# Optimization experiments

Hardware: AMD Instinct MI355X
Metric: run time of the kernel (lower is better)

Reference implementation:

```python
import jax, jax.numpy as jnp
import numpy as np

N_NODES = 100000
N_EDGES = 800000
IN_DIM, HID_DIM, OUT_DIM = 128, 256, 40


def setup_inputs() -> dict:
    key = jax.random.key(0)
    ks = jax.random.split(key, 8)
    x = jax.random.normal(ks[0], (N_NODES, IN_DIM), dtype=jnp.float32)
    edge_index = jax.random.randint(ks[1], (2, N_EDGES), 0, N_NODES, dtype=jnp.int64)
    # PyG SAGEConv params: lin_l (neighbor path, with bias), lin_r (root path, no bias)
    def glorot(k, fan_in, fan_out):
        lim = np.sqrt(6.0 / (fan_in + fan_out)).astype(np.float32)
        return jax.random.uniform(k, (fan_in, fan_out), jnp.float32, -lim, lim)
    W1l = glorot(ks[2], IN_DIM, HID_DIM)
    W1r = glorot(ks[3], IN_DIM, HID_DIM)
    b1 = jnp.zeros((HID_DIM,), jnp.float32)
    W2l = glorot(ks[4], HID_DIM, OUT_DIM)
    W2r = glorot(ks[5], HID_DIM, OUT_DIM)
    b2 = jnp.zeros((OUT_DIM,), jnp.float32)
    return {"x": x, "edge_index": edge_index, "W1l": W1l, "b1": b1, "W1r": W1r,
            "W2l": W2l, "b2": b2, "W2r": W2r}


def _sage_conv(x, src, dst, Wl, b, Wr, n_nodes):
    # mean aggregation of neighbor features: gather x[src], scatter-add to dst, divide by degree
    msg = x[src]                                              # [E, D]
    agg = jax.ops.segment_sum(msg, dst, num_segments=n_nodes)  # [N, D]
    cnt = jax.ops.segment_sum(jnp.ones((src.shape[0],), x.dtype), dst,
                              num_segments=n_nodes)            # [N]
    agg = agg / jnp.maximum(cnt, 1.0)[:, None]
    # out = lin_l(mean_agg) + lin_r(x)  (lin_l carries the bias in PyG)
    return agg @ Wl + b + x @ Wr


def reference(x, edge_index, W1l, b1, W1r, W2l, b2, W2r):
    src, dst = edge_index[0], edge_index[1]
    n = x.shape[0]
    h = _sage_conv(x, src, dst, W1l, b1, W1r, n)
    h = jax.nn.relu(h)
    # F.dropout(training=self.training): identity at inference
    out = _sage_conv(h, src, dst, W2l, b2, W2r, n)
    return out
```

## Files before the change

kernel.cpp:

```cpp
#include <hip/hip_runtime.h>
#include <hip/hip_bf16.h>


#define NN   100000
#define NNP  100096
#define NE   800000
#define NB1  391
#define NCHK 32
#define ECH  25000
#define NSLI 16
#define NSL  6250

typedef unsigned short ushortT;
typedef __attribute__((ext_vector_type(8))) short bf16x8;
typedef __attribute__((ext_vector_type(4))) float f32x4;

__device__ __forceinline__ unsigned short f2b(float f) {
    unsigned u = __float_as_uint(f);
    return (unsigned short)((u + 0x7fffu + ((u >> 16) & 1u)) >> 16);
}
__device__ __forceinline__ float b2f(unsigned short v) {
    return __uint_as_float(((unsigned)v) << 16);
}
__device__ __forceinline__ void llds16(const unsigned short* g, unsigned short* s) {
    __builtin_amdgcn_global_load_lds(
        (const __attribute__((address_space(1))) void*)g,
        (__attribute__((address_space(3))) void*)s, 16, 0, 0);
}

__global__ __launch_bounds__(256) void k_prep(
        const float* __restrict__ x,
        const float* __restrict__ W1l, const float* __restrict__ W1r,
        const float* __restrict__ W2l, const float* __restrict__ W2r,
        ushortT* __restrict__ Ac, ushortT* __restrict__ WT1,
        ushortT* __restrict__ WT2,
        const int* __restrict__ dst, int* __restrict__ deg32) {
    __shared__ int hist[NSL];
    int bid = blockIdx.x;
    if (bid < 12500) {
        int t = bid * 256 + threadIdx.x;
        int row = t >> 5, c4 = t & 31;
        float4 v = *(const float4*)&x[(size_t)row * 128 + c4 * 4];
        ushortT* p = Ac + (size_t)row * 256 + 128 + c4 * 4;
        p[0] = f2b(v.x); p[1] = f2b(v.y); p[2] = f2b(v.z); p[3] = f2b(v.w);

        if (t < 65536) {
            int n = t >> 8, k = t & 255;
            float w = (k < 128) ? W1l[(size_t)k * 256 + n]
                                : W1r[(size_t)(k - 128) * 256 + n];
            WT1[t] = f2b(w);
        } else if (t < 65536 + 20480) {
            int j = t - 65536;
            int n = j >> 8, k = j & 255;
            float w = (n < 40) ? W2l[(size_t)k * 40 + n]
                               : W2r[(size_t)k * 40 + (n - 40)];
            WT2[j] = f2b(w);
        }
    } else {
        int idx = bid - 12500;
        int s = idx & (NSLI - 1), c = idx >> 4;
        for (int i = threadIdx.x; i < NSL; i += 256) hist[i] = 0;
        __syncthreads();
        int e0 = c * ECH, lo = s * NSL;
        for (int i = threadIdx.x; i < ECH; i += 1024) {
            int d[4];
            bool m[4];
#pragma unroll
            for (int u = 0; u < 4; ++u) {
                int ii = i + u * 256;
                m[u] = ii < ECH;
                d[u] = dst[e0 + (m[u] ? ii : 0)];
            }
#pragma unroll
            for (int u = 0; u < 4; ++u) {
                unsigned dd = (unsigned)(d[u] - lo);
                if (m[u] && dd < (unsigned)NSL) atomicAdd(&hist[dd], 1);
            }
        }
        __syncthreads();
        for (int i = threadIdx.x; i < NSL; i += 256)
            deg32[c * NN + lo + i] = hist[i];
    }
}

__global__ __launch_bounds__(256) void k_scan1(const int* __restrict__ deg32,
                                               int* __restrict__ rp,
                                               int* __restrict__ rpp,
                                               int* __restrict__ bsum) {
    __shared__ int s[256];
    int t = threadIdx.x;
    int i = blockIdx.x * 256 + t;
    int d32[NCHK];
    int v = 0;
#pragma unroll
    for (int r = 0; r < NCHK; ++r) {
        d32[r] = (i < NN) ? deg32[r * NN + i] : 0;
        v += d32[r];
    }
    s[t] = v;
    __syncthreads();
    for (int off = 1; off < 256; off <<= 1) {
        int add = (t >= off) ? s[t - off] : 0;
        __syncthreads();
        s[t] += add;
        __syncthreads();
    }
    int ex = s[t] - v;
    if (i <= NN) rp[i] = ex;
    if (i < NN) {
        int run = ex;
#pragma unroll
        for (int r = 0; r < NCHK; ++r) {
            rpp[r * NN + i] = run;
            run += d32[r];
        }
    }
    if (t == 255) bsum[blockIdx.x] = s[255];
}

__global__ __launch_bounds__(512) void k_scan2(int* __restrict__ bsum) {
    __shared__ int s[512];
    int t = threadIdx.x;
    int v = (t < NB1) ? bsum[t] : 0;
    s[t] = v;
    __syncthreads();
    for (int off = 1; off < 512; off <<= 1) {
        int add = (t >= off) ? s[t - off] : 0;
        __syncthreads();
        s[t] += add;
        __syncthreads();
    }
    if (t < NB1) bsum[t] = s[t] - v;
}

__global__ __launch_bounds__(256) void k_fillB(const int* __restrict__ src,
                                               const int* __restrict__ dst,
                                               const int* __restrict__ rpp,
                                               const int* __restrict__ bsum,
                                               int* __restrict__ col) {
    __shared__ int off[NSL];
    int s = blockIdx.x & (NSLI - 1), c = blockIdx.x >> 4;
    int lo = s * NSL;
    for (int i = threadIdx.x; i < NSL; i += 256)
        off[i] = bsum[(lo + i) >> 8] + rpp[c * NN + lo + i];
    __syncthreads();
    int e0 = c * ECH;
    for (int i = threadIdx.x; i < ECH; i += 1024) {
        int d[4], sv[4];
        bool m[4];
#pragma unroll
        for (int u = 0; u < 4; ++u) {
            int ii = i + u * 256;
            m[u] = ii < ECH;
            int e = e0 + (m[u] ? ii : 0);
            d[u] = dst[e];
            sv[u] = src[e];
        }
#pragma unroll
        for (int u = 0; u < 4; ++u) {
            unsigned dd = (unsigned)(d[u] - lo);
            if (m[u] && dd < (unsigned)NSL) {
                int k = atomicAdd(&off[dd], 1);
                col[k] = sv[u];
            }
        }
    }
}

__global__ __launch_bounds__(256) void k_agg1(const int* __restrict__ rp,
                                              const int* __restrict__ bsum,
                                              const int* __restrict__ col,
                                              ushortT* __restrict__ Ac) {
    int node = blockIdx.x * 4 + (threadIdx.x >> 6);
    int l = threadIdx.x & 63;
    if (node >= NN) return;
    int seg = l >> 4, dl = l & 15;
    int beg = rp[node] + bsum[node >> 8];
    int end = rp[node + 1] + bsum[(node + 1) >> 8];
    int deg = end - beg;
    float a[8] = {0.f, 0.f, 0.f, 0.f, 0.f, 0.f, 0.f, 0.f};
    for (int base = 0; base < deg; base += 64) {
        int cnt = min(64, deg - base);
        int cv = col[beg + base + min(l, cnt - 1)];
        for (int j = 0; j < cnt; j += 16) {
            int e[4], idx[4];
            bf16x8 v[4];
#pragma unroll
            for (int u = 0; u < 4; ++u) {
                e[u] = j + u * 4 + seg;
                idx[u] = __shfl(cv, min(e[u], cnt - 1));
            }
#pragma unroll
            for (int u = 0; u < 4; ++u) {
                v[u] = (bf16x8){0, 0, 0, 0, 0, 0, 0, 0};
                if (e[u] < cnt)
                    v[u] = *(const bf16x8*)(Ac + (size_t)idx[u] * 256 + 128 + dl * 8);
            }
#pragma unroll
            for (int u = 0; u < 4; ++u)
#pragma unroll
                for (int i = 0; i < 8; ++i)
                    a[i] += b2f((unsigned short)v[u][i]);
        }
    }
#pragma unroll
    for (int i = 0; i < 8; ++i) {
        a[i] += __shfl_xor(a[i], 16);
        a[i] += __shfl_xor(a[i], 32);
    }
    if (seg == 0) {
        float inv = 1.0f / fmaxf((float)deg, 1.0f);
        bf16x8 o;
#pragma unroll
        for (int i = 0; i < 8; ++i) o[i] = (short)f2b(a[i] * inv);
        *(bf16x8*)(Ac + (size_t)node * 256 + dl * 8) = o;
    }
}

#define HSP 264
__global__ __launch_bounds__(256, 3) void k_fused(
        const ushortT* __restrict__ Ac, const ushortT* __restrict__ WT1,
        const float* __restrict__ b1, const ushortT* __restrict__ WT2,
        const float* __restrict__ b2, ushortT* __restrict__ y2,
        ushortT* __restrict__ t) {
    __shared__ ushortT As[64 * 64];
    __shared__ ushortT Bs[64 * HSP];
    const int tid = threadIdx.x, l = tid & 63, wid = tid >> 6;
    const int m0 = blockIdx.x * 64;
    const int q = l >> 4, r = l & 15;
    const int swz = (l & 7) ^ ((l >> 3) & 7);

    f32x4 acc[4][4];
#pragma unroll
    for (int i = 0; i < 4; ++i)
#pragma unroll
        for (int j = 0; j < 4; ++j) acc[i][j] = (f32x4){0.f, 0.f, 0.f, 0.f};

    for (int kt = 0; kt < 256; kt += 64) {
#pragma unroll
        for (int i = 0; i < 2; ++i) {
            int flat = wid * 2 + i;
            int row = flat * 8 + (l >> 3);
            llds16(Ac + (size_t)(m0 + row) * 256 + kt + swz * 8, &As[flat * 512]);
        }
#pragma unroll
        for (int i = 0; i < 8; ++i) {
            int flat = wid * 8 + i;
            int row = flat * 8 + (l >> 3);
            llds16(WT1 + (size_t)row * 256 + kt + swz * 8, &Bs[flat * 512]);
        }
        __syncthreads();
#pragma unroll
        for (int ks = 0; ks < 64; ks += 32) {
            bf16x8 af[4], bfr[4];
            const int cs = (((ks >> 3) + q) ^ (r & 7)) * 8;
#pragma unroll
            for (int mt = 0; mt < 4; ++mt)
                af[mt] = *(const bf16x8*)&As[(mt * 16 + r) * 64 + cs];
#pragma unroll
            for (int nt = 0; nt < 4; ++nt)
                bfr[nt] = *(const bf16x8*)&Bs[(wid * 64 + nt * 16 + r) * 64 + cs];
#pragma unroll
            for (int mt = 0; mt < 4; ++mt)
#pragma unroll
                for (int nt = 0; nt < 4; ++nt)
                    acc[mt][nt] = __builtin_amdgcn_mfma_f32_16x16x32_bf16(
                        af[mt], bfr[nt], acc[mt][nt], 0, 0, 0);
        }
        __syncthreads();
    }
#pragma unroll
    for (int nt = 0; nt < 4; ++nt) {
        int colb = wid * 64 + nt * 16 + r;
        float bb = b1[colb];
#pragma unroll
        for (int mt = 0; mt < 4; ++mt) {
            int rowb = mt * 16 + q * 4;
#pragma unroll
            for (int j = 0; j < 4; ++j)
                Bs[(rowb + j) * HSP + colb] = f2b(fmaxf(acc[mt][nt][j] + bb, 0.f));
        }
    }
    __syncthreads();

    f32x4 acc2[2][4];
#pragma unroll
    for (int i = 0; i < 2; ++i)
#pragma unroll
        for (int j = 0; j < 4; ++j) acc2[i][j] = (f32x4){0.f, 0.f, 0.f, 0.f};
#pragma unroll
    for (int kk = 0; kk < 256; kk += 32) {
        bf16x8 af[4];
#pragma unroll
        for (int mt = 0; mt < 4; ++mt)
            af[mt] = *(const bf16x8*)&Bs[(mt * 16 + r) * HSP + kk + q * 8];
#pragma unroll
        for (int cc = 0; cc < 2; ++cc) {
            int ct = wid + cc * 4;
            if (ct < 5) {
                bf16x8 bq = *(const bf16x8*)(WT2 + (size_t)(ct * 16 + r) * 256 + kk + q * 8);
#pragma unroll
                for (int mt = 0; mt < 4; ++mt)
                    acc2[cc][mt] = __builtin_amdgcn_mfma_f32_16x16x32_bf16(
                        af[mt], bq, acc2[cc][mt], 0, 0, 0);
            }
        }
    }
#pragma unroll
    for (int cc = 0; cc < 2; ++cc) {
        int ct = wid + cc * 4;
        if (ct >= 5) continue;
        int c = ct * 16 + r;
        float bb = (c >= 40) ? b2[c - 40] : 0.f;
#pragma unroll
        for (int mt = 0; mt < 4; ++mt) {
            int row0 = m0 + mt * 16 + q * 4;
#pragma unroll
            for (int j = 0; j < 4; ++j) {
                float v = acc2[cc][mt][j];
                if (c < 40)
                    y2[(size_t)(row0 + j) * 40 + c] = f2b(v);
                else
                    t[(size_t)(row0 + j) * 40 + (c - 40)] = f2b(v + bb);
            }
        }
    }
}

__global__ __launch_bounds__(256) void k_agg2(const int* __restrict__ rp,
                                              const int* __restrict__ bsum,
                                              const int* __restrict__ col,
                                              const ushortT* __restrict__ y2,
                                              const ushortT* __restrict__ t,
                                              float* __restrict__ out) {
    int node = blockIdx.x * 4 + (threadIdx.x >> 6);
    int l = threadIdx.x & 63;
    if (node >= NN) return;
    int seg = l >> 4, dl = l & 15;
    int beg = rp[node] + bsum[node >> 8];
    int end = rp[node + 1] + bsum[(node + 1) >> 8];
    int deg = end - beg;
    bool act = dl < 10;
    float a0 = 0.f, a1 = 0.f, a2 = 0.f, a3 = 0.f;
    for (int base = 0; base < deg; base += 64) {
        int cnt = min(64, deg - base);
        int cv = col[beg + base + min(l, cnt - 1)];
        for (int j = 0; j < cnt; j += 16) {
            int e[4], idx[4];
            ushort4 v[4];
#pragma unroll
            for (int u = 0; u < 4; ++u) {
                e[u] = j + u * 4 + seg;
                idx[u] = __shfl(cv, min(e[u], cnt - 1));
            }
#pragma unroll
            for (int u = 0; u < 4; ++u) {
                v[u] = (ushort4){0, 0, 0, 0};
                if (e[u] < cnt && act)
                    v[u] = *(const ushort4*)(y2 + (size_t)idx[u] * 40 + dl * 4);
            }
#pragma unroll
            for (int u = 0; u < 4; ++u) {
                a0 += b2f(v[u].x);
                a1 += b2f(v[u].y);
                a2 += b2f(v[u].z);
                a3 += b2f(v[u].w);
            }
        }
    }
    a0 += __shfl_xor(a0, 16); a0 += __shfl_xor(a0, 32);
    a1 += __shfl_xor(a1, 16); a1 += __shfl_xor(a1, 32);
    a2 += __shfl_xor(a2, 16); a2 += __shfl_xor(a2, 32);
    a3 += __shfl_xor(a3, 16); a3 += __shfl_xor(a3, 32);
    if (seg == 0 && act) {
        float inv = 1.0f / fmaxf((float)deg, 1.0f);
        size_t o = (size_t)node * 40 + dl * 4;
        ushort4 tv = *(const ushort4*)&t[o];
        float4 ov;
        ov.x = a0 * inv + b2f(tv.x);
        ov.y = a1 * inv + b2f(tv.y);
        ov.z = a2 * inv + b2f(tv.z);
        ov.w = a3 * inv + b2f(tv.w);
        *(float4*)&out[o] = ov;
    }
}

extern "C" void kernel_launch(void* const* d_in, const int* in_sizes, int n_in,
                              void* d_out, int out_size, void* d_ws, size_t ws_size,
                              hipStream_t stream) {
    const float* x   = (const float*)d_in[0];
    const int*   ei  = (const int*)d_in[1];
    const int*   src = ei;
    const int*   dst = ei + NE;
    const float* W1l = (const float*)d_in[2];
    const float* b1  = (const float*)d_in[3];
    const float* W1r = (const float*)d_in[4];
    const float* W2l = (const float*)d_in[5];
    const float* b2  = (const float*)d_in[6];
    const float* W2r = (const float*)d_in[7];
    float* out = (float*)d_out;

    size_t off = 0;
    char* base = (char*)d_ws;
    auto alloc = [&](size_t bytes) -> void* {
        void* p = base + off;
        off += (bytes + 255) & ~(size_t)255;
        return p;
    };
    int*     deg32 = (int*)alloc((size_t)NCHK * NN * 4);
    int*     rp    = (int*)alloc((size_t)(NN + 1) * 4);
    int*     rpp   = (int*)alloc((size_t)NCHK * NN * 4);
    int*     col   = (int*)alloc((size_t)NE * 4);
    int*     bsum  = (int*)alloc(512 * 4);
    ushortT* Ac    = (ushortT*)alloc((size_t)NNP * 256 * 2);
    ushortT* y2    = (ushortT*)alloc((size_t)NNP * 40 * 2);
    ushortT* t     = (ushortT*)alloc((size_t)NNP * 40 * 2);
    ushortT* WT1   = (ushortT*)alloc(256 * 256 * 2);
    ushortT* WT2   = (ushortT*)alloc(80 * 256 * 2);

    k_prep<<<12500 + NCHK * NSLI, 256, 0, stream>>>(x, W1l, W1r, W2l, W2r,
                                                    Ac, WT1, WT2, dst, deg32);
    k_scan1<<<NB1, 256, 0, stream>>>(deg32, rp, rpp, bsum);
    k_scan2<<<1, 512, 0, stream>>>(bsum);
    k_fillB<<<NCHK * NSLI, 256, 0, stream>>>(src, dst, rpp, bsum, col);
    k_agg1<<<(NN + 3) / 4, 256, 0, stream>>>(rp, bsum, col, Ac);
    k_fused<<<NNP / 64, 256, 0, stream>>>(Ac, WT1, b1, WT2, b2, y2, t);
    k_agg2<<<(NN + 3) / 4, 256, 0, stream>>>(rp, bsum, col, y2, t, out);
}
```

Before: 266.5 us.

## Load GEMM fragments directly from global memory instead of staging through LDS

The first GEMM in the fused kernel stops staging A and W tiles into shared memory with global_load_lds and syncthreads. Each lane now loads its bf16x8 MFMA fragments straight from global memory across a fully unrolled K loop. This frees the As buffer, so the occupancy hint rises from 3 to 4 blocks. The prep kernel also writes the bf16 conversion of x as one 8-byte vector store instead of four scalar stores. The trade-off is that every wave now fetches the shared weight and A rows itself through the cache, with no LDS reuse and with strided 16-byte accesses.

```diff
diff --git a/kernel.cpp b/kernel.cpp
--- a/kernel.cpp
+++ b/kernel.cpp
@@ -21,11 +21,6 @@
 }
 __device__ __forceinline__ float b2f(unsigned short v) {
     return __uint_as_float(((unsigned)v) << 16);
-}
-__device__ __forceinline__ void llds16(const unsigned short* g, unsigned short* s) {
-    __builtin_amdgcn_global_load_lds(
-        (const __attribute__((address_space(1))) void*)g,
-        (__attribute__((address_space(3))) void*)s, 16, 0, 0);
 }
 
 __global__ __launch_bounds__(256) void k_prep(
@@ -41,8 +36,9 @@
         int t = bid * 256 + threadIdx.x;
         int row = t >> 5, c4 = t & 31;
         float4 v = *(const float4*)&x[(size_t)row * 128 + c4 * 4];
-        ushortT* p = Ac + (size_t)row * 256 + 128 + c4 * 4;
-        p[0] = f2b(v.x); p[1] = f2b(v.y); p[2] = f2b(v.z); p[3] = f2b(v.w);
+        ushort4 o;
+        o.x = f2b(v.x); o.y = f2b(v.y); o.z = f2b(v.z); o.w = f2b(v.w);
+        *(ushort4*)(Ac + (size_t)row * 256 + 128 + c4 * 4) = o;
 
         if (t < 65536) {
             int n = t >> 8, k = t & 255;
@@ -218,17 +214,15 @@
 }
 
 #define HSP 264
-__global__ __launch_bounds__(256, 3) void k_fused(
+__global__ __launch_bounds__(256, 4) void k_fused(
         const ushortT* __restrict__ Ac, const ushortT* __restrict__ WT1,
         const float* __restrict__ b1, const ushortT* __restrict__ WT2,
         const float* __restrict__ b2, ushortT* __restrict__ y2,
         ushortT* __restrict__ t) {
-    __shared__ ushortT As[64 * 64];
     __shared__ ushortT Bs[64 * HSP];
     const int tid = threadIdx.x, l = tid & 63, wid = tid >> 6;
     const int m0 = blockIdx.x * 64;
     const int q = l >> 4, r = l & 15;
-    const int swz = (l & 7) ^ ((l >> 3) & 7);
 
     f32x4 acc[4][4];
 #pragma unroll
@@ -236,39 +230,25 @@
 #pragma unroll
         for (int j = 0; j < 4; ++j) acc[i][j] = (f32x4){0.f, 0.f, 0.f, 0.f};
 
-    for (int kt = 0; kt < 256; kt += 64) {
-#pragma unroll
-        for (int i = 0; i < 2; ++i) {
-            int flat = wid * 2 + i;
-            int row = flat * 8 + (l >> 3);
-            llds16(Ac + (size_t)(m0 + row) * 256 + kt + swz * 8, &As[flat * 512]);
-        }
-#pragma unroll
-        for (int i = 0; i < 8; ++i) {
-            int flat = wid * 8 + i;
-            int row = flat * 8 + (l >> 3);
-            llds16(WT1 + (size_t)row * 256 + kt + swz * 8, &Bs[flat * 512]);
-        }
-        __syncthreads();
-#pragma unroll
-        for (int ks = 0; ks < 64; ks += 32) {
-            bf16x8 af[4], bfr[4];
-            const int cs = (((ks >> 3) + q) ^ (r & 7)) * 8;
-#pragma unroll
-            for (int mt = 0; mt < 4; ++mt)
-                af[mt] = *(const bf16x8*)&As[(mt * 16 + r) * 64 + cs];
+    const ushortT* aBase = Ac + (size_t)(m0 + r) * 256 + q * 8;
+    const ushortT* bBase = WT1 + (size_t)(wid * 64 + r) * 256 + q * 8;
+#pragma unroll
+    for (int kk = 0; kk < 256; kk += 32) {
+        bf16x8 af[4], bfr[4];
+#pragma unroll
+        for (int mt = 0; mt < 4; ++mt)
+            af[mt] = *(const bf16x8*)(aBase + (size_t)mt * 16 * 256 + kk);
+#pragma unroll
+        for (int nt = 0; nt < 4; ++nt)
+            bfr[nt] = *(const bf16x8*)(bBase + (size_t)nt * 16 * 256 + kk);
+#pragma unroll
+        for (int mt = 0; mt < 4; ++mt)
 #pragma unroll
             for (int nt = 0; nt < 4; ++nt)
-                bfr[nt] = *(const bf16x8*)&Bs[(wid * 64 + nt * 16 + r) * 64 + cs];
-#pragma unroll
-            for (int mt = 0; mt < 4; ++mt)
-#pragma unroll
-                for (int nt = 0; nt < 4; ++nt)
-                    acc[mt][nt] = __builtin_amdgcn_mfma_f32_16x16x32_bf16(
-                        af[mt], bfr[nt], acc[mt][nt], 0, 0, 0);
-        }
-        __syncthreads();
-    }
+                acc[mt][nt] = __builtin_amdgcn_mfma_f32_16x16x32_bf16(
+                    af[mt], bfr[nt], acc[mt][nt], 0, 0, 0);
+    }
+
 #pragma unroll
     for (int nt = 0; nt < 4; ++nt) {
         int colb = wid * 64 + nt * 16 + r;
```

New measurement: 299.3 us. +12.3%, slower.

## Pre-swizzle weights into MFMA fragment order and load B directly from global

Applied to the files above, without the earlier changes.

The weight matrices are now written during prep in an MFMA-fragment-major layout, so each lane in the fused GEMM reads its B operand with one coalesced 16-byte global load instead of staging WT1 through LDS. The whole 64x256 A tile is loaded into LDS once, reusing the existing Bs buffer, which removes the per-k-tile barriers and the separate As array. The x-to-bf16 store in prep is also vectorized. The intent is less LDS traffic and fewer syncs, at the cost of repeated global/L2 reads of weights by every block.

```diff
diff --git a/kernel.cpp b/kernel.cpp
--- a/kernel.cpp
+++ b/kernel.cpp
@@ -27,13 +27,17 @@
         (const __attribute__((address_space(1))) void*)g,
         (__attribute__((address_space(3))) void*)s, 16, 0, 0);
 }
+__device__ __forceinline__ int fragIdx(int n, int k) {
+    return (((n >> 4) * 8 + (k >> 5)) * 64 + ((k >> 3) & 3) * 16 + (n & 15)) * 8
+           + (k & 7);
+}
 
 __global__ __launch_bounds__(256) void k_prep(
         const float* __restrict__ x,
         const float* __restrict__ W1l, const float* __restrict__ W1r,
         const float* __restrict__ W2l, const float* __restrict__ W2r,
-        ushortT* __restrict__ Ac, ushortT* __restrict__ WT1,
-        ushortT* __restrict__ WT2,
+        ushortT* __restrict__ Ac, ushortT* __restrict__ WT1f,
+        ushortT* __restrict__ WT2f,
         const int* __restrict__ dst, int* __restrict__ deg32) {
     __shared__ int hist[NSL];
     int bid = blockIdx.x;
@@ -41,20 +45,21 @@
         int t = bid * 256 + threadIdx.x;
         int row = t >> 5, c4 = t & 31;
         float4 v = *(const float4*)&x[(size_t)row * 128 + c4 * 4];
-        ushortT* p = Ac + (size_t)row * 256 + 128 + c4 * 4;
-        p[0] = f2b(v.x); p[1] = f2b(v.y); p[2] = f2b(v.z); p[3] = f2b(v.w);
+        ushort4 o;
+        o.x = f2b(v.x); o.y = f2b(v.y); o.z = f2b(v.z); o.w = f2b(v.w);
+        *(ushort4*)(Ac + (size_t)row * 256 + 128 + c4 * 4) = o;
 
         if (t < 65536) {
             int n = t >> 8, k = t & 255;
             float w = (k < 128) ? W1l[(size_t)k * 256 + n]
                                 : W1r[(size_t)(k - 128) * 256 + n];
-            WT1[t] = f2b(w);
+            WT1f[fragIdx(n, k)] = f2b(w);
         } else if (t < 65536 + 20480) {
             int j = t - 65536;
             int n = j >> 8, k = j & 255;
             float w = (n < 40) ? W2l[(size_t)k * 40 + n]
                                : W2r[(size_t)k * 40 + (n - 40)];
-            WT2[j] = f2b(w);
+            WT2f[fragIdx(n, k)] = f2b(w);
         }
     } else {
         int idx = bid - 12500;
@@ -219,56 +224,55 @@
 
 #define HSP 264
 __global__ __launch_bounds__(256, 3) void k_fused(
-        const ushortT* __restrict__ Ac, const ushortT* __restrict__ WT1,
-        const float* __restrict__ b1, const ushortT* __restrict__ WT2,
+        const ushortT* __restrict__ Ac, const ushortT* __restrict__ WT1f,
+        const float* __restrict__ b1, const ushortT* __restrict__ WT2f,
         const float* __restrict__ b2, ushortT* __restrict__ y2,
         ushortT* __restrict__ t) {
-    __shared__ ushortT As[64 * 64];
     __shared__ ushortT Bs[64 * HSP];
     const int tid = threadIdx.x, l = tid & 63, wid = tid >> 6;
     const int m0 = blockIdx.x * 64;
     const int q = l >> 4, r = l & 15;
     const int swz = (l & 7) ^ ((l >> 3) & 7);
 
-    f32x4 acc[4][4];
-#pragma unroll
-    for (int i = 0; i < 4; ++i)
-#pragma unroll
-        for (int j = 0; j < 4; ++j) acc[i][j] = (f32x4){0.f, 0.f, 0.f, 0.f};
-
-    for (int kt = 0; kt < 256; kt += 64) {
+#pragma unroll
+    for (int ktc = 0; ktc < 4; ++ktc)
 #pragma unroll
         for (int i = 0; i < 2; ++i) {
             int flat = wid * 2 + i;
             int row = flat * 8 + (l >> 3);
-            llds16(Ac + (size_t)(m0 + row) * 256 + kt + swz * 8, &As[flat * 512]);
-        }
-#pragma unroll
-        for (int i = 0; i < 8; ++i) {
-            int flat = wid * 8 + i;
-            int row = flat * 8 + (l >> 3);
-            llds16(WT1 + (size_t)row * 256 + kt + swz * 8, &Bs[flat * 512]);
-        }
-        __syncthreads();
-#pragma unroll
-        for (int ks = 0; ks < 64; ks += 32) {
-            bf16x8 af[4], bfr[4];
-            const int cs = (((ks >> 3) + q) ^ (r & 7)) * 8;
-#pragma unroll
-            for (int mt = 0; mt < 4; ++mt)
-                af[mt] = *(const bf16x8*)&As[(mt * 16 + r) * 64 + cs];
+            llds16(Ac + (size_t)(m0 + row) * 256 + ktc * 64 + swz * 8,
+                   &Bs[ktc * 4096 + flat * 512]);
+        }
+
+    f32x4 acc[4][4];
+#pragma unroll
+    for (int i = 0; i < 4; ++i)
+#pragma unroll
+        for (int j = 0; j < 4; ++j) acc[i][j] = (f32x4){0.f, 0.f, 0.f, 0.f};
+
+    __syncthreads();
+
+    const ushortT* bBase = WT1f + (size_t)(wid * 4 * 8) * 512 + l * 8;
+#pragma unroll
+    for (int kk = 0; kk < 256; kk += 32) {
+        const int ktc = kk >> 6, ks = kk & 63, kc = kk >> 5;
+        const int cs = (((ks >> 3) + q) ^ (r & 7)) * 8;
+        bf16x8 af[4], bfr[4];
+#pragma unroll
+        for (int mt = 0; mt < 4; ++mt)
+            af[mt] = *(const bf16x8*)&Bs[ktc * 4096 + (mt * 16 + r) * 64 + cs];
+#pragma unroll
+        for (int nt = 0; nt < 4; ++nt)
+            bfr[nt] = *(const bf16x8*)(bBase + (size_t)(nt * 8 + kc) * 512);
+#pragma unroll
+        for (int mt = 0; mt < 4; ++mt)
 #pragma unroll
             for (int nt = 0; nt < 4; ++nt)
-                bfr[nt] = *(const bf16x8*)&Bs[(wid * 64 + nt * 16 + r) * 64 + cs];
-#pragma unroll
-            for (int mt = 0; mt < 4; ++mt)
-#pragma unroll
-                for (int nt = 0; nt < 4; ++nt)
-                    acc[mt][nt] = __builtin_amdgcn_mfma_f32_16x16x32_bf16(
-                        af[mt], bfr[nt], acc[mt][nt], 0, 0, 0);
-        }
-        __syncthreads();
-    }
+                acc[mt][nt] = __builtin_amdgcn_mfma_f32_16x16x32_bf16(
+                    af[mt], bfr[nt], acc[mt][nt], 0, 0, 0);
+    }
+    __syncthreads();
+
 #pragma unroll
     for (int nt = 0; nt < 4; ++nt) {
         int colb = wid * 64 + nt * 16 + r;
@@ -298,7 +302,8 @@
         for (int cc = 0; cc < 2; ++cc) {
             int ct = wid + cc * 4;
             if (ct < 5) {
-                bf16x8 bq = *(const bf16x8*)(WT2 + (size_t)(ct * 16 + r) * 256 + kk + q * 8);
+                bf16x8 bq = *(const bf16x8*)(WT2f
+                        + (size_t)(ct * 8 + (kk >> 5)) * 512 + l * 8);
 #pragma unroll
                 for (int mt = 0; mt < 4; ++mt)
                     acc2[cc][mt] = __builtin_amdgcn_mfma_f32_16x16x32_bf16(
@@ -415,15 +420,15 @@
     ushortT* Ac    = (ushortT*)alloc((size_t)NNP * 256 * 2);
     ushortT* y2    = (ushortT*)alloc((size_t)NNP * 40 * 2);
     ushortT* t     = (ushortT*)alloc((size_t)NNP * 40 * 2);
-    ushortT* WT1   = (ushortT*)alloc(256 * 256 * 2);
-    ushortT* WT2   = (ushortT*)alloc(80 * 256 * 2);
+    ushortT* WT1f  = (ushortT*)alloc(256 * 256 * 2);
+    ushortT* WT2f  = (ushortT*)alloc(80 * 256 * 2);
 
     k_prep<<<12500 + NCHK * NSLI, 256, 0, stream>>>(x, W1l, W1r, W2l, W2r,
-                                                    Ac, WT1, WT2, dst, deg32);
+                                                    Ac, WT1f, WT2f, dst, deg32);
     k_scan1<<<NB1, 256, 0, stream>>>(deg32, rp, rpp, bsum);
     k_scan2<<<1, 512, 0, stream>>>(bsum);
     k_fillB<<<NCHK * NSLI, 256, 0, stream>>>(src, dst, rpp, bsum, col);
     k_agg1<<<(NN + 3) / 4, 256, 0, stream>>>(rp, bsum, col, Ac);
-    k_fused<<<NNP / 64, 256, 0, stream>>>(Ac, WT1, b1, WT2, b2, y2, t);
+    k_fused<<<NNP / 64, 256, 0, stream>>>(Ac, WT1f, b1, WT2f, b2, y2, t);
     k_agg2<<<(NN + 3) / 4, 256, 0, stream>>>(rp, bsum, col, y2, t, out);
 }
```

Measured after the change: 272.0 us. 1.02x slower.
